# Kernel tuning notes

Measured on AMD Instinct MI355X. Metric: run time of the kernel, lower is better.

## Reference

```python
import jax, jax.numpy as jnp
import numpy as np
import math

IN_F, OUT_F = 512, 512
N_HEADS, N_SPLITS = 32, 4
N = 1024
DELTA_SCALE = 0.1


def setup_inputs() -> dict:
    key = jax.random.key(0)
    k_x, k_h, k_s, k_w = jax.random.split(key, 4)
    stdv = 1.0 / math.sqrt(OUT_F)
    inputs = {
        "input": jax.random.normal(k_x, (N, IN_F), dtype=jnp.float32),
        "head_ix": jax.random.randint(k_h, (N,), 0, N_HEADS, dtype=jnp.int32),
        "split_ix": jax.random.randint(k_s, (N,), 0, N_SPLITS, dtype=jnp.int32),
        # learned parameters (EmbeddingTensor tables)
        "weight": jax.random.uniform(k_w, (N_HEADS, IN_F, OUT_F), dtype=jnp.float32,
                                     minval=-stdv, maxval=stdv),
        "delta_weight": jnp.zeros((N_HEADS * N_SPLITS, IN_F, OUT_F), dtype=jnp.float32),
        "bias": jnp.zeros((N_HEADS, OUT_F), dtype=jnp.float32),
    }
    return inputs


def reference(input, head_ix, split_ix, weight, delta_weight, bias):
    # per-sample weight: base[head] + 0.1 * delta[head * n_splits + split]
    w = weight[head_ix] + delta_weight[head_ix * N_SPLITS + split_ix] * DELTA_SCALE  # [N, in, out]
    # batched vector-matrix multiply + per-head bias
    return jnp.einsum('ab,abc->ac', input, w) + bias[head_ix]  # [N, out]
```

## Files before the change

kernel.cpp:

```cpp
#include <hip/hip_runtime.h>

#define N_SAMP   1024
#define IN_F     512
#define OUT_F    512
#define N_HEADS  32
#define N_SPLITS 4
#define N_GROUPS (N_HEADS * N_SPLITS)
#define DELTA_SCALE 0.1f


typedef float f32x2 __attribute__((ext_vector_type(2)));

__device__ __forceinline__ f32x2 nt_load2(const float* p) {
    return __builtin_nontemporal_load((const f32x2*)p);
}
__device__ __forceinline__ void nt_store2(float* p, f32x2 v) {
    __builtin_nontemporal_store(v, (f32x2*)p);
}

__global__ __launch_bounds__(256, 4) void lms_fused_nt(
    const float* __restrict__ X, const int* __restrict__ head_ix,
    const int* __restrict__ split_ix, const float* __restrict__ W,
    const float* __restrict__ D, const float* __restrict__ bias,
    float* __restrict__ out)
{
    constexpr int J    = 16;
    constexpr int KQ   = 8;
    constexpr int KT   = IN_F / KQ;
    constexpr int NST  = KT / 4;
    constexpr int NOUT = (J * 32) / 256;

    __shared__ float buf[J * IN_F];
    __shared__ int   list[N_SAMP];
    __shared__ int   wsum[4];

    const int g    = blockIdx.y;
    const int h    = g >> 2;
    const int c0   = blockIdx.x * 64;
    const int tid  = threadIdx.x;
    const int c2   = tid & 31;
    const int kq   = tid >> 5;
    const int lane = tid & 63;
    const int wave = tid >> 6;

    int run = 0;
    for (int r = 0; r < N_SAMP / 256; ++r) {
        const int i   = r * 256 + tid;
        const int key = head_ix[i] * N_SPLITS + split_ix[i];
        const bool hit = (key == g);
        const unsigned long long m = __ballot(hit);
        if (lane == 0) wsum[wave] = __popcll(m);
        __syncthreads();
        int base = run;
        for (int w = 0; w < 4; ++w)
            if (w < wave) base += wsum[w];
        if (hit)
            list[base + __popcll(m & ((1ULL << lane) - 1ULL))] = i;
        run += wsum[0] + wsum[1] + wsum[2] + wsum[3];
        __syncthreads();
    }
    const int total = run;
    if (total == 0) return;

    const size_t roff = (size_t)(kq * KT) * OUT_F + c0 + c2 * 2;
    const float* wp = W + (size_t)h * (IN_F * OUT_F) + roff;
    const float* dp = D + (size_t)g * (IN_F * OUT_F) + roff;

    for (int s0 = 0; s0 < total; s0 += J) {
        const int nc = min(total - s0, J);

        __syncthreads();
        for (int i = tid; i < J * (IN_F / 4); i += 256) {
            const int s = i >> 7, q = i & 127;
            float4 v = make_float4(0.f, 0.f, 0.f, 0.f);
            if (s < nc)
                v = *(const float4*)(X + (size_t)list[s0 + s] * IN_F + q * 4);
            *(float4*)(&buf[s * IN_F + q * 4]) = v;
        }
        __syncthreads();

        float2 acc[J];
#pragma unroll
        for (int j = 0; j < J; ++j) { acc[j].x = 0.f; acc[j].y = 0.f; }

        float2 wb[2][4];
        f32x2  db[2][4];
#pragma unroll
        for (int u = 0; u < 4; ++u) {
            wb[0][u] = *(const float2*)(wp + (size_t)u * OUT_F);
            db[0][u] = nt_load2(dp + (size_t)u * OUT_F);
        }

#pragma unroll 2
        for (int st = 0; st < NST; ++st) {
            const int nx = (st + 1 < NST) ? st + 1 : NST - 1;
            const int nb = (st + 1) & 1, cb = st & 1;
            const float* wn = wp + (size_t)(nx * 4) * OUT_F;
            const float* dn = dp + (size_t)(nx * 4) * OUT_F;
#pragma unroll
            for (int u = 0; u < 4; ++u) {
                wb[nb][u] = *(const float2*)(wn + (size_t)u * OUT_F);
                db[nb][u] = nt_load2(dn + (size_t)u * OUT_F);
            }

            float2 rc[4];
#pragma unroll
            for (int u = 0; u < 4; ++u) {
                rc[u].x = wb[cb][u].x + DELTA_SCALE * db[cb][u].x;
                rc[u].y = wb[cb][u].y + DELTA_SCALE * db[cb][u].y;
            }

            const float* xb = &buf[kq * KT + st * 4];
#pragma unroll
            for (int j = 0; j < J; ++j) {
                const float4 xv = *(const float4*)(xb + j * IN_F);
                acc[j].x += xv.x * rc[0].x; acc[j].y += xv.x * rc[0].y;
                acc[j].x += xv.y * rc[1].x; acc[j].y += xv.y * rc[1].y;
                acc[j].x += xv.z * rc[2].x; acc[j].y += xv.z * rc[2].y;
                acc[j].x += xv.w * rc[3].x; acc[j].y += xv.w * rc[3].y;
            }
        }

        __syncthreads();
        float2* Red = (float2*)buf;
#pragma unroll
        for (int j = 0; j < J; ++j)
            Red[(kq * J + j) * 32 + c2] = acc[j];
        __syncthreads();

#pragma unroll
        for (int t = 0; t < NOUT; ++t) {
            const int oi = t * 256 + tid;
            const int j = oi >> 5, cc = oi & 31;
            if (j < nc) {
                float2 s = make_float2(0.f, 0.f);
#pragma unroll
                for (int q = 0; q < KQ; ++q) {
                    const float2 r = Red[(q * J + j) * 32 + cc];
                    s.x += r.x; s.y += r.y;
                }
                const float2 bv =
                    *(const float2*)(bias + (size_t)h * OUT_F + c0 + cc * 2);
                float* op = out + (size_t)list[s0 + j] * OUT_F + c0 + cc * 2;
                f32x2 res;
                res.x = s.x + bv.x;
                res.y = s.y + bv.y;
                nt_store2(op, res);
            }
        }
    }
}

extern "C" void kernel_launch(void* const* d_in, const int* in_sizes, int n_in,
                              void* d_out, int out_size, void* d_ws, size_t ws_size,
                              hipStream_t stream) {
    const float* X        = (const float*)d_in[0];
    const int*   head_ix  = (const int*)d_in[1];
    const int*   split_ix = (const int*)d_in[2];
    const float* W        = (const float*)d_in[3];
    const float* D        = (const float*)d_in[4];
    const float* bias     = (const float*)d_in[5];
    float*       out      = (float*)d_out;

    dim3 gf(OUT_F / 64, N_GROUPS);
    lms_fused_nt<<<gf, 256, 0, stream>>>(X, head_ix, split_ix, W, D, bias, out);
}
```

Measured before the change: 237.7 us.

## Use 512-thread blocks with 16-way K split and two-pass reduction

```diff
diff --git a/kernel.cpp b/kernel.cpp
--- a/kernel.cpp
+++ b/kernel.cpp
@@ -18,21 +18,20 @@
     __builtin_nontemporal_store(v, (f32x2*)p);
 }
 
-__global__ __launch_bounds__(256, 4) void lms_fused_nt(
+__global__ __launch_bounds__(512, 8) void lms_fused_nt512(
     const float* __restrict__ X, const int* __restrict__ head_ix,
     const int* __restrict__ split_ix, const float* __restrict__ W,
     const float* __restrict__ D, const float* __restrict__ bias,
     float* __restrict__ out)
 {
     constexpr int J    = 16;
-    constexpr int KQ   = 8;
+    constexpr int KQ   = 16;
     constexpr int KT   = IN_F / KQ;
     constexpr int NST  = KT / 4;
-    constexpr int NOUT = (J * 32) / 256;
 
     __shared__ float buf[J * IN_F];
     __shared__ int   list[N_SAMP];
-    __shared__ int   wsum[4];
+    __shared__ int   wsum[8];
 
     const int g    = blockIdx.y;
     const int h    = g >> 2;
@@ -44,19 +43,23 @@
     const int wave = tid >> 6;
 
     int run = 0;
-    for (int r = 0; r < N_SAMP / 256; ++r) {
-        const int i   = r * 256 + tid;
+    for (int r = 0; r < N_SAMP / 512; ++r) {
+        const int i   = r * 512 + tid;
         const int key = head_ix[i] * N_SPLITS + split_ix[i];
         const bool hit = (key == g);
         const unsigned long long m = __ballot(hit);
         if (lane == 0) wsum[wave] = __popcll(m);
         __syncthreads();
         int base = run;
-        for (int w = 0; w < 4; ++w)
+#pragma unroll
+        for (int w = 0; w < 8; ++w)
             if (w < wave) base += wsum[w];
         if (hit)
             list[base + __popcll(m & ((1ULL << lane) - 1ULL))] = i;
-        run += wsum[0] + wsum[1] + wsum[2] + wsum[3];
+        int rs = 0;
+#pragma unroll
+        for (int w = 0; w < 8; ++w) rs += wsum[w];
+        run += rs;
         __syncthreads();
     }
     const int total = run;
@@ -70,7 +73,9 @@
         const int nc = min(total - s0, J);
 
         __syncthreads();
-        for (int i = tid; i < J * (IN_F / 4); i += 256) {
+#pragma unroll
+        for (int f = 0; f < 4; ++f) {
+            const int i = f * 512 + tid;
             const int s = i >> 7, q = i & 127;
             float4 v = make_float4(0.f, 0.f, 0.f, 0.f);
             if (s < nc)
@@ -121,31 +126,33 @@
             }
         }
 
-        __syncthreads();
         float2* Red = (float2*)buf;
 #pragma unroll
-        for (int j = 0; j < J; ++j)
-            Red[(kq * J + j) * 32 + c2] = acc[j];
-        __syncthreads();
-
+        for (int hf = 0; hf < 2; ++hf) {
+            __syncthreads();
 #pragma unroll
-        for (int t = 0; t < NOUT; ++t) {
-            const int oi = t * 256 + tid;
-            const int j = oi >> 5, cc = oi & 31;
-            if (j < nc) {
-                float2 s = make_float2(0.f, 0.f);
+            for (int jj = 0; jj < 8; ++jj)
+                Red[(kq * 8 + jj) * 32 + c2] = acc[hf * 8 + jj];
+            __syncthreads();
+            if (tid < 256) {
+                const int j  = tid >> 5;
+                const int cc = tid & 31;
+                const int js = hf * 8 + j;
+                if (js < nc) {
+                    float2 s = make_float2(0.f, 0.f);
 #pragma unroll
-                for (int q = 0; q < KQ; ++q) {
-                    const float2 r = Red[(q * J + j) * 32 + cc];
-                    s.x += r.x; s.y += r.y;
+                    for (int q = 0; q < KQ; ++q) {
+                        const float2 r = Red[(q * 8 + j) * 32 + cc];
+                        s.x += r.x; s.y += r.y;
+                    }
+                    const float2 bv =
+                        *(const float2*)(bias + (size_t)h * OUT_F + c0 + cc * 2);
+                    float* op = out + (size_t)list[s0 + js] * OUT_F + c0 + cc * 2;
+                    f32x2 res;
+                    res.x = s.x + bv.x;
+                    res.y = s.y + bv.y;
+                    nt_store2(op, res);
                 }
-                const float2 bv =
-                    *(const float2*)(bias + (size_t)h * OUT_F + c0 + cc * 2);
-                float* op = out + (size_t)list[s0 + j] * OUT_F + c0 + cc * 2;
-                f32x2 res;
-                res.x = s.x + bv.x;
-                res.y = s.y + bv.y;
-                nt_store2(op, res);
             }
         }
     }
@@ -163,5 +170,5 @@
     float*       out      = (float*)d_out;
 
     dim3 gf(OUT_F / 64, N_GROUPS);
-    lms_fused_nt<<<gf, 256, 0, stream>>>(X, head_ix, split_ix, W, D, bias, out);
+    lms_fused_nt512<<<gf, 512, 0, stream>>>(X, head_ix, split_ix, W, D, bias, out);
 }
```

Result: slower. 463.1 us (+94.8%).
